# Kernel tuning notes

Measured on AMD Instinct MI355X. Metric: run time of the kernel, lower is better.

Reference implementation:

```python
import jax, jax.numpy as jnp
import numpy as np

B, N, E, H = 16, 512, 256, 8
ALPHA = 0.2  # leaky relu negative slope


def setup_inputs() -> dict:
    key = jax.random.key(0)
    k1, k2, k3, k4, k5, k6 = jax.random.split(key, 6)
    x = jax.random.normal(k1, (B, N, E), dtype=jnp.float32)
    A = (jax.random.uniform(k2, (B, N, N)) < 0.3).astype(jnp.float32)
    s = 1.0 / np.sqrt(E)
    W = jax.random.uniform(k3, (E, E), minval=-s, maxval=s, dtype=jnp.float32)
    bW = jax.random.uniform(k4, (E,), minval=-s, maxval=s, dtype=jnp.float32)
    a = jax.random.uniform(k5, (E, 2 * H), minval=-s, maxval=s, dtype=jnp.float32)
    ba = jax.random.uniform(k6, (2 * H,), minval=-s, maxval=s, dtype=jnp.float32)
    return {"x": x, "A": A, "W": W, "bW": bW, "a": a, "ba": ba}


def reference(x, A, W, bW, a, ba):
    # Wh = W(x): [B, N, E]
    Wh = jnp.einsum("bne,ef->bnf", x, W) + bW
    # attention coefficients: a(Wh) -> [B, N, 2H] -> [B, H, N, 2]
    e12 = (jnp.einsum("bne,eh->bnh", Wh, a) + ba).reshape(B, N, H, 2).transpose(0, 2, 1, 3)
    e = e12[..., 0:1] + jnp.swapaxes(e12[..., 1:2], -2, -1)  # [B, H, N, N]
    # split heads: [B, H, N, D]
    Whh = Wh.reshape(B, N, H, E // H).transpose(0, 2, 1, 3)
    mask = A[:, None, :, :] > 0.5  # [B, H(bcast), N, N]
    neg = jnp.finfo(e.dtype).min
    score = jnp.where(mask, jax.nn.leaky_relu(e, ALPHA), neg)
    att = jax.nn.softmax(score, axis=-1)
    # rows with no neighbors: torch softmax(-inf row) -> nan -> nan_to_num -> 0
    has_nbr = jnp.any(mask, axis=-1, keepdims=True)
    att = jnp.where(has_nbr, att, 0.0)
    out = jnp.einsum("bhij,bhjd->bhid", att, Whh)  # [B, H, N, D]
    out = out.transpose(0, 2, 1, 3).reshape(B, N, E)
    # dropout is identity in eval/reference mode
    return jax.nn.relu(out)
```

## Files before the change

### kernel.cpp

```cpp
#include <hip/hip_runtime.h>
#include <math.h>

#define Bv 16
#define Nv 512
#define Ev 256
#define Hv 8
#define Dv 32
#define LOG2E 1.44269504088896340736f

typedef _Float16 half8 __attribute__((ext_vector_type(8)));
typedef _Float16 half4_t __attribute__((ext_vector_type(4)));
typedef float f32x4 __attribute__((ext_vector_type(4)));

__global__ __launch_bounds__(256) void prep_kernel(const float* __restrict__ W,
                                                   const float* __restrict__ aP,
                                                   const float* __restrict__ bW,
                                                   const float* __restrict__ ba,
                                                   const float* __restrict__ A,
                                                   _Float16* __restrict__ WT,
                                                   float* __restrict__ Wa,
                                                   float* __restrict__ cba,
                                                   unsigned int* __restrict__ Abm) {
    __shared__ float t[32][33];
    const int tid = threadIdx.x;
    const int blk = blockIdx.x;

    if (blk < 64) {
        const int k0 = (blk >> 3) * 32, n0 = (blk & 7) * 32;
        *(float4*)&t[tid >> 3][(tid & 7) * 4] =
            *(const float4*)&W[(size_t)(k0 + (tid >> 3)) * Ev + n0 + (tid & 7) * 4];
        __syncthreads();
        const int nn = tid >> 3, kg = (tid & 7) * 4;
        half4_t hv;
        hv[0] = (_Float16)t[kg + 0][nn];
        hv[1] = (_Float16)t[kg + 1][nn];
        hv[2] = (_Float16)t[kg + 2][nn];
        hv[3] = (_Float16)t[kg + 3][nn];
        *(half4_t*)&WT[(size_t)(n0 + nn) * Ev + k0 + kg] = hv;
    } else if (blk < 80) {
        const int e = (blk - 64) * 16 + (tid >> 4);
        const int c = tid & 15;
        float dot = 0.f;
        for (int k4 = 0; k4 < 64; ++k4) {
            float4 wv = *(const float4*)&W[(size_t)e * Ev + k4 * 4];
            dot += wv.x * aP[(k4 * 4 + 0) * 16 + c];
            dot += wv.y * aP[(k4 * 4 + 1) * 16 + c];
            dot += wv.z * aP[(k4 * 4 + 2) * 16 + c];
            dot += wv.w * aP[(k4 * 4 + 3) * 16 + c];
        }
        Wa[e * 16 + c] = dot;
    } else if (blk == 80) {
        if (tid < 16) {
            float d = ba[tid];
            for (int k = 0; k < Ev; ++k) d += bW[k] * aP[k * 16 + tid];
            cba[tid] = d;
        }
    } else {
        const int ablk = blk - 81;
        const int w = tid >> 6, lane = tid & 63;
        const size_t base = (size_t)ablk * 2048 + w * 512;
        #pragma unroll
        for (int r = 0; r < 8; ++r) {
            const size_t f = base + r * 64 + lane;
            const bool pred = A[f] > 0.5f;
            unsigned long long m = __ballot(pred);
            if (lane == 0) *(unsigned long long*)&Abm[f >> 5] = m;
        }
    }
}

__global__ __launch_bounds__(256) void whT_gemm(const float* __restrict__ x,
                                                const _Float16* __restrict__ WT,
                                                const float* __restrict__ bW,
                                                _Float16* __restrict__ WhT) {
    __shared__ _Float16 xs[64][40];
    __shared__ _Float16 wsT[64][40];
    __shared__ _Float16 ldsTr[64][72];

    const int tid = threadIdx.x;
    const int m0 = blockIdx.x * 64;
    const int n0 = blockIdx.y * 64;
    const int w = tid >> 6;
    const int lane = tid & 63;
    const int row = lane & 15;
    const int strip = lane >> 4;

    f32x4 acc[4] = {{0.f, 0.f, 0.f, 0.f}, {0.f, 0.f, 0.f, 0.f},
                    {0.f, 0.f, 0.f, 0.f}, {0.f, 0.f, 0.f, 0.f}};

    const int sr = tid >> 2;
    const int skg = (tid & 3) * 8;

    for (int k0 = 0; k0 < Ev; k0 += 32) {
        {
            const float* xp = &x[(size_t)(m0 + sr) * Ev + k0 + skg];
            float4 v0 = *(const float4*)xp;
            float4 v1 = *(const float4*)(xp + 4);
            half8 hv;
            hv[0] = (_Float16)v0.x; hv[1] = (_Float16)v0.y;
            hv[2] = (_Float16)v0.z; hv[3] = (_Float16)v0.w;
            hv[4] = (_Float16)v1.x; hv[5] = (_Float16)v1.y;
            hv[6] = (_Float16)v1.z; hv[7] = (_Float16)v1.w;
            *(half8*)&xs[sr][skg] = hv;
        }
        {
            half8 hv = *(const half8*)&WT[(size_t)(n0 + sr) * Ev + k0 + skg];
            *(half8*)&wsT[sr][skg] = hv;
        }
        __syncthreads();

        half8 af = *(const half8*)&xs[w * 16 + row][strip * 8];
        #pragma unroll
        for (int ns = 0; ns < 4; ++ns) {
            half8 bf = *(const half8*)&wsT[ns * 16 + row][strip * 8];
            acc[ns] = __builtin_amdgcn_mfma_f32_16x16x32_f16(af, bf, acc[ns], 0, 0, 0);
        }
        __syncthreads();
    }

    #pragma unroll
    for (int ns = 0; ns < 4; ++ns) {
        const float bias = bW[n0 + ns * 16 + row];
        half4_t hv;
        hv[0] = (_Float16)(acc[ns][0] + bias);
        hv[1] = (_Float16)(acc[ns][1] + bias);
        hv[2] = (_Float16)(acc[ns][2] + bias);
        hv[3] = (_Float16)(acc[ns][3] + bias);
        *(half4_t*)&ldsTr[ns * 16 + row][w * 16 + strip * 4] = hv;
    }
    __syncthreads();

    {
        const int n = tid >> 2, jg = tid & 3;
        uint4 v0 = *(const uint4*)&ldsTr[n][jg * 16];
        uint4 v1 = *(const uint4*)&ldsTr[n][jg * 16 + 8];
        const int ng = n0 + n;
        const int h = ng >> 5, d = ng & 31;
        const int b = m0 >> 9, j0 = m0 & 511;
        _Float16* dst = &WhT[(((size_t)b * Hv + h) * Dv + d) * Nv + j0 + jg * 16];
        *(uint4*)dst = v0;
        *(uint4*)(dst + 8) = v1;
    }
}

__global__ __launch_bounds__(256) void e12_kernel(const float* __restrict__ x,
                                                  const float* __restrict__ Wa,
                                                  const float* __restrict__ cba,
                                                  float* __restrict__ e1,
                                                  float* __restrict__ e2) {
    __shared__ float WaS[Ev][16];
    __shared__ float cbaS[16];

    const int tid = threadIdx.x;
    const int m0 = blockIdx.x * 32;

    #pragma unroll
    for (int u = 0; u < 4; ++u) {
        int f = tid + u * 256;
        *(float4*)&WaS[f >> 2][(f & 3) * 4] = *(const float4*)&Wa[f * 4];
    }
    if (tid < 16) cbaS[tid] = cba[tid];
    __syncthreads();

    const int r = tid >> 3;
    const int q = (tid >> 1) & 3;
    const int kh = tid & 1;
    const int m = m0 + r;

    const float* xr = &x[(size_t)m * Ev + kh * 128];
    float4 acc = {0.f, 0.f, 0.f, 0.f};

    #pragma unroll 8
    for (int it = 0; it < 32; ++it) {
        float4 xv = *(const float4*)&xr[it * 4];
        const int kb = kh * 128 + it * 4;
        float4 w0 = *(const float4*)&WaS[kb + 0][q * 4];
        float4 w1 = *(const float4*)&WaS[kb + 1][q * 4];
        float4 w2 = *(const float4*)&WaS[kb + 2][q * 4];
        float4 w3 = *(const float4*)&WaS[kb + 3][q * 4];
        acc.x += xv.x * w0.x + xv.y * w1.x + xv.z * w2.x + xv.w * w3.x;
        acc.y += xv.x * w0.y + xv.y * w1.y + xv.z * w2.y + xv.w * w3.y;
        acc.z += xv.x * w0.z + xv.y * w1.z + xv.z * w2.z + xv.w * w3.z;
        acc.w += xv.x * w0.w + xv.y * w1.w + xv.z * w2.w + xv.w * w3.w;
    }

    acc.x += __shfl_xor(acc.x, 1);
    acc.y += __shfl_xor(acc.y, 1);
    acc.z += __shfl_xor(acc.z, 1);
    acc.w += __shfl_xor(acc.w, 1);

    if (kh == 0) {
        const int b = m >> 9, i = m & 511;
        #pragma unroll
        for (int cc = 0; cc < 4; ++cc) {
            const int c = q * 4 + cc;
            const float val = ((cc == 0) ? acc.x : (cc == 1) ? acc.y : (cc == 2) ? acc.z : acc.w)
                              + cbaS[c];
            const int h = c >> 1;
            float* dst = (c & 1) ? e2 : e1;
            dst[(((b << 3) + h) << 9) + i] = val;
        }
    }
}

__global__ __launch_bounds__(256) void attn_kernel(const unsigned int* __restrict__ Abm,
                                                   const _Float16* __restrict__ WhT,
                                                   const float* __restrict__ e1g,
                                                   const float* __restrict__ e2g,
                                                   float* __restrict__ out) {
    __shared__ _Float16 whT[Dv * Nv];
    __shared__ float E2pS[Nv];
    __shared__ float E2nS[Nv];

    const int tid = threadIdx.x;
    const int i0 = blockIdx.x * 64;
    const int h = blockIdx.y;
    const int b = blockIdx.z;
    const int bh = (b << 3) + h;

    const _Float16* src = WhT + (size_t)bh * (Dv * Nv);
    #pragma unroll
    for (int u = 0; u < 8; ++u) {
        int f = tid + u * 256;
        int d = f >> 6, blk = f & 63;
        uint4 v = *(const uint4*)(src + d * Nv + blk * 8);
        *(uint4*)&whT[d * Nv + ((blk ^ (d & 7)) * 8)] = v;
    }
    {
        float ea = e2g[(bh << 9) + tid] * LOG2E;
        E2pS[tid] = __builtin_amdgcn_exp2f(ea);
        E2nS[tid] = __builtin_amdgcn_exp2f(0.2f * ea);
        float eb = e2g[(bh << 9) + tid + 256] * LOG2E;
        E2pS[tid + 256] = __builtin_amdgcn_exp2f(eb);
        E2nS[tid + 256] = __builtin_amdgcn_exp2f(0.2f * eb);
    }
    __syncthreads();

    const int w = tid >> 6;
    const int lane = tid & 63;
    const int row = lane & 15;
    const int strip = lane >> 4;
    const int i = i0 + (w << 4) + row;

    const float e1v = e1g[(bh << 9) + i] * LOG2E;
    const float E1p = __builtin_amdgcn_exp2f(e1v);
    const float E1n = __builtin_amdgcn_exp2f(0.2f * e1v);

    const uint4* bmp = (const uint4*)&Abm[((size_t)b * Nv + i) << 4];
    const uint4 bm0 = bmp[0], bm1 = bmp[1], bm2 = bmp[2], bm3 = bmp[3];
    const unsigned int dwarr[16] = {bm0.x, bm0.y, bm0.z, bm0.w,
                                    bm1.x, bm1.y, bm1.z, bm1.w,
                                    bm2.x, bm2.y, bm2.z, bm2.w,
                                    bm3.x, bm3.y, bm3.z, bm3.w};
    const int sh = strip << 3;

    const int d0 = lane & 15;
    const int sw = d0 & 7;
    const _Float16* brow0 = &whT[d0 * Nv];
    const _Float16* brow1 = &whT[(16 + d0) * Nv];

    f32x4 acc0 = {0.f, 0.f, 0.f, 0.f};
    f32x4 acc1 = {0.f, 0.f, 0.f, 0.f};
    float denom = 0.f;

    #pragma unroll
    for (int t = 0; t < 16; ++t) {
        const unsigned int byte_ = (dwarr[t] >> sh) & 0xFFu;
        const float4 p0 = *(const float4*)&E2pS[t * 32 + sh];
        const float4 p1 = *(const float4*)&E2pS[t * 32 + sh + 4];
        const float4 n0 = *(const float4*)&E2nS[t * 32 + sh];
        const float4 n1 = *(const float4*)&E2nS[t * 32 + sh + 4];

        const float q0 = (byte_ & 1u)   ? fmaxf(E1p * p0.x, E1n * n0.x) : 0.f;
        const float q1 = (byte_ & 2u)   ? fmaxf(E1p * p0.y, E1n * n0.y) : 0.f;
        const float q2 = (byte_ & 4u)   ? fmaxf(E1p * p0.z, E1n * n0.z) : 0.f;
        const float q3 = (byte_ & 8u)   ? fmaxf(E1p * p0.w, E1n * n0.w) : 0.f;
        const float q4 = (byte_ & 16u)  ? fmaxf(E1p * p1.x, E1n * n1.x) : 0.f;
        const float q5 = (byte_ & 32u)  ? fmaxf(E1p * p1.y, E1n * n1.y) : 0.f;
        const float q6 = (byte_ & 64u)  ? fmaxf(E1p * p1.z, E1n * n1.z) : 0.f;
        const float q7 = (byte_ & 128u) ? fmaxf(E1p * p1.w, E1n * n1.w) : 0.f;

        denom += ((q0 + q1) + (q2 + q3)) + ((q4 + q5) + (q6 + q7));

        half8 af;
        af[0] = (_Float16)q0; af[1] = (_Float16)q1;
        af[2] = (_Float16)q2; af[3] = (_Float16)q3;
        af[4] = (_Float16)q4; af[5] = (_Float16)q5;
        af[6] = (_Float16)q6; af[7] = (_Float16)q7;

        const int blk = ((t << 2) + strip) ^ sw;
        half8 b0 = *(const half8*)(brow0 + blk * 8);
        half8 b1 = *(const half8*)(brow1 + blk * 8);
        acc0 = __builtin_amdgcn_mfma_f32_16x16x32_f16(af, b0, acc0, 0, 0, 0);
        acc1 = __builtin_amdgcn_mfma_f32_16x16x32_f16(af, b1, acc1, 0, 0, 0);
    }

    denom += __shfl_xor(denom, 16);
    denom += __shfl_xor(denom, 32);

    #pragma unroll
    for (int e = 0; e < 4; ++e) {
        const float dn = __shfl(denom, (strip << 2) + e);
        const float rv = (dn > 0.f) ? (1.f / dn) : 0.f;
        const int orow = i0 + (w << 4) + (strip << 2) + e;
        float* orp = &out[((size_t)b * Nv + orow) * Ev + (h << 5)];
        orp[d0] = fmaxf(acc0[e] * rv, 0.f);
        orp[16 + d0] = fmaxf(acc1[e] * rv, 0.f);
    }
}

extern "C" void kernel_launch(void* const* d_in, const int* in_sizes, int n_in,
                              void* d_out, int out_size, void* d_ws, size_t ws_size,
                              hipStream_t stream) {
    const float* x  = (const float*)d_in[0];
    const float* A  = (const float*)d_in[1];
    const float* W  = (const float*)d_in[2];
    const float* bW = (const float*)d_in[3];
    const float* a  = (const float*)d_in[4];
    const float* ba = (const float*)d_in[5];
    float* out = (float*)d_out;

    char* ws = (char*)d_ws;
    _Float16* WT  = (_Float16*)ws;
    float*    Wa  = (float*)(ws + 131072);
    float*    cba = (float*)(ws + 131072 + 16384);
    _Float16* WhT = (_Float16*)(ws + 131072 + 16384 + 256);
    float*    e1  = (float*)(ws + 131072 + 16384 + 256 + 4194304);
    float*    e2  = e1 + (size_t)Bv * Hv * Nv;
    unsigned int* Abm = (unsigned int*)(e2 + (size_t)Bv * Hv * Nv);

    prep_kernel<<<2129, 256, 0, stream>>>(W, a, bW, ba, A, WT, Wa, cba, Abm);
    whT_gemm<<<dim3(Bv * Nv / 64, Ev / 64), 256, 0, stream>>>(x, WT, bW, WhT);
    e12_kernel<<<dim3(Bv * Nv / 32), 256, 0, stream>>>(x, Wa, cba, e1, e2);
    attn_kernel<<<dim3(Nv / 64, Hv, Bv), 256, 0, stream>>>(Abm, WhT, e1, e2, out);
}
```

Measured before the change: 45.27 us.

## Fuse W transpose and Wh GEMM into prep kernel; double rows per attention wave

Merges the separate weight-transpose and Wh GEMM launches into one fused prep kernel. Each GEMM block now loads and transposes its 256x64 slice of W straight into LDS as fp16, which removes one kernel launch and the WT round trip through global memory. The attention kernel now gives each wave 32 rows instead of 16, so the staged WhT tile and E2 values are reused across twice as many rows with half as many blocks. The cost is a larger LDS footprint and redundant W reads in the prep kernel, more registers in attention, and lower block count and occupancy.

```diff
diff --git a/kernel.cpp b/kernel.cpp
--- a/kernel.cpp
+++ b/kernel.cpp
@@ -12,33 +12,96 @@
 typedef _Float16 half4_t __attribute__((ext_vector_type(4)));
 typedef float f32x4 __attribute__((ext_vector_type(4)));
 
-__global__ __launch_bounds__(256) void prep_kernel(const float* __restrict__ W,
-                                                   const float* __restrict__ aP,
-                                                   const float* __restrict__ bW,
-                                                   const float* __restrict__ ba,
-                                                   const float* __restrict__ A,
-                                                   _Float16* __restrict__ WT,
-                                                   float* __restrict__ Wa,
-                                                   float* __restrict__ cba,
-                                                   unsigned int* __restrict__ Abm) {
-    __shared__ float t[32][33];
+__global__ __launch_bounds__(256) void fused_pre(const float* __restrict__ x,
+                                                 const float* __restrict__ W,
+                                                 const float* __restrict__ bW,
+                                                 const float* __restrict__ aP,
+                                                 const float* __restrict__ ba,
+                                                 const float* __restrict__ A,
+                                                 _Float16* __restrict__ WhT,
+                                                 float* __restrict__ Wa,
+                                                 float* __restrict__ cba,
+                                                 unsigned int* __restrict__ Abm) {
+    __shared__ _Float16 Wp[64][264];
+    __shared__ _Float16 xs[64][40];
+    __shared__ _Float16 ldsTr[64][72];
+
     const int tid = threadIdx.x;
     const int blk = blockIdx.x;
 
-    if (blk < 64) {
-        const int k0 = (blk >> 3) * 32, n0 = (blk & 7) * 32;
-        *(float4*)&t[tid >> 3][(tid & 7) * 4] =
-            *(const float4*)&W[(size_t)(k0 + (tid >> 3)) * Ev + n0 + (tid & 7) * 4];
+    if (blk < 512) {
+        const int m0 = (blk >> 2) * 64;
+        const int n0 = (blk & 3) * 64;
+        const int w = tid >> 6;
+        const int lane = tid & 63;
+        const int row = lane & 15;
+        const int strip = lane >> 4;
+
+        {
+            const float* wrow = &W[(size_t)tid * Ev + n0];
+            #pragma unroll
+            for (int u = 0; u < 16; ++u) {
+                float4 v = *(const float4*)&wrow[u * 4];
+                Wp[u * 4 + 0][tid] = (_Float16)v.x;
+                Wp[u * 4 + 1][tid] = (_Float16)v.y;
+                Wp[u * 4 + 2][tid] = (_Float16)v.z;
+                Wp[u * 4 + 3][tid] = (_Float16)v.w;
+            }
+        }
+
+        f32x4 acc[4] = {{0.f, 0.f, 0.f, 0.f}, {0.f, 0.f, 0.f, 0.f},
+                        {0.f, 0.f, 0.f, 0.f}, {0.f, 0.f, 0.f, 0.f}};
+        const int sr = tid >> 2;
+        const int skg = (tid & 3) * 8;
+
+        for (int k0 = 0; k0 < Ev; k0 += 32) {
+            {
+                const float* xp = &x[(size_t)(m0 + sr) * Ev + k0 + skg];
+                float4 v0 = *(const float4*)xp;
+                float4 v1 = *(const float4*)(xp + 4);
+                half8 hv;
+                hv[0] = (_Float16)v0.x; hv[1] = (_Float16)v0.y;
+                hv[2] = (_Float16)v0.z; hv[3] = (_Float16)v0.w;
+                hv[4] = (_Float16)v1.x; hv[5] = (_Float16)v1.y;
+                hv[6] = (_Float16)v1.z; hv[7] = (_Float16)v1.w;
+                *(half8*)&xs[sr][skg] = hv;
+            }
+            __syncthreads();
+
+            half8 af = *(const half8*)&xs[w * 16 + row][strip * 8];
+            #pragma unroll
+            for (int ns = 0; ns < 4; ++ns) {
+                half8 bf = *(const half8*)&Wp[ns * 16 + row][k0 + strip * 8];
+                acc[ns] = __builtin_amdgcn_mfma_f32_16x16x32_f16(af, bf, acc[ns], 0, 0, 0);
+            }
+            __syncthreads();
+        }
+
+        #pragma unroll
+        for (int ns = 0; ns < 4; ++ns) {
+            const float bias = bW[n0 + ns * 16 + row];
+            half4_t hv;
+            hv[0] = (_Float16)(acc[ns][0] + bias);
+            hv[1] = (_Float16)(acc[ns][1] + bias);
+            hv[2] = (_Float16)(acc[ns][2] + bias);
+            hv[3] = (_Float16)(acc[ns][3] + bias);
+            *(half4_t*)&ldsTr[ns * 16 + row][w * 16 + strip * 4] = hv;
+        }
         __syncthreads();
-        const int nn = tid >> 3, kg = (tid & 7) * 4;
-        half4_t hv;
-        hv[0] = (_Float16)t[kg + 0][nn];
-        hv[1] = (_Float16)t[kg + 1][nn];
-        hv[2] = (_Float16)t[kg + 2][nn];
-        hv[3] = (_Float16)t[kg + 3][nn];
-        *(half4_t*)&WT[(size_t)(n0 + nn) * Ev + k0 + kg] = hv;
-    } else if (blk < 80) {
-        const int e = (blk - 64) * 16 + (tid >> 4);
+
+        {
+            const int n = tid >> 2, jg = tid & 3;
+            uint4 v0 = *(const uint4*)&ldsTr[n][jg * 16];
+            uint4 v1 = *(const uint4*)&ldsTr[n][jg * 16 + 8];
+            const int ng = n0 + n;
+            const int h = ng >> 5, d = ng & 31;
+            const int b = m0 >> 9, j0 = m0 & 511;
+            _Float16* dst = &WhT[(((size_t)b * Hv + h) * Dv + d) * Nv + j0 + jg * 16];
+            *(uint4*)dst = v0;
+            *(uint4*)(dst + 8) = v1;
+        }
+    } else if (blk < 528) {
+        const int e = (blk - 512) * 16 + (tid >> 4);
         const int c = tid & 15;
         float dot = 0.f;
         for (int k4 = 0; k4 < 64; ++k4) {
@@ -49,14 +112,14 @@
             dot += wv.w * aP[(k4 * 4 + 3) * 16 + c];
         }
         Wa[e * 16 + c] = dot;
-    } else if (blk == 80) {
+    } else if (blk == 528) {
         if (tid < 16) {
             float d = ba[tid];
             for (int k = 0; k < Ev; ++k) d += bW[k] * aP[k * 16 + tid];
             cba[tid] = d;
         }
     } else {
-        const int ablk = blk - 81;
+        const int ablk = blk - 529;
         const int w = tid >> 6, lane = tid & 63;
         const size_t base = (size_t)ablk * 2048 + w * 512;
         #pragma unroll
@@ -66,80 +129,6 @@
             unsigned long long m = __ballot(pred);
             if (lane == 0) *(unsigned long long*)&Abm[f >> 5] = m;
         }
-    }
-}
-
-__global__ __launch_bounds__(256) void whT_gemm(const float* __restrict__ x,
-                                                const _Float16* __restrict__ WT,
-                                                const float* __restrict__ bW,
-                                                _Float16* __restrict__ WhT) {
-    __shared__ _Float16 xs[64][40];
-    __shared__ _Float16 wsT[64][40];
-    __shared__ _Float16 ldsTr[64][72];
-
-    const int tid = threadIdx.x;
-    const int m0 = blockIdx.x * 64;
-    const int n0 = blockIdx.y * 64;
-    const int w = tid >> 6;
-    const int lane = tid & 63;
-    const int row = lane & 15;
-    const int strip = lane >> 4;
-
-    f32x4 acc[4] = {{0.f, 0.f, 0.f, 0.f}, {0.f, 0.f, 0.f, 0.f},
-                    {0.f, 0.f, 0.f, 0.f}, {0.f, 0.f, 0.f, 0.f}};
-
-    const int sr = tid >> 2;
-    const int skg = (tid & 3) * 8;
-
-    for (int k0 = 0; k0 < Ev; k0 += 32) {
-        {
-            const float* xp = &x[(size_t)(m0 + sr) * Ev + k0 + skg];
-            float4 v0 = *(const float4*)xp;
-            float4 v1 = *(const float4*)(xp + 4);
-            half8 hv;
-            hv[0] = (_Float16)v0.x; hv[1] = (_Float16)v0.y;
-            hv[2] = (_Float16)v0.z; hv[3] = (_Float16)v0.w;
-            hv[4] = (_Float16)v1.x; hv[5] = (_Float16)v1.y;
-            hv[6] = (_Float16)v1.z; hv[7] = (_Float16)v1.w;
-            *(half8*)&xs[sr][skg] = hv;
-        }
-        {
-            half8 hv = *(const half8*)&WT[(size_t)(n0 + sr) * Ev + k0 + skg];
-            *(half8*)&wsT[sr][skg] = hv;
-        }
-        __syncthreads();
-
-        half8 af = *(const half8*)&xs[w * 16 + row][strip * 8];
-        #pragma unroll
-        for (int ns = 0; ns < 4; ++ns) {
-            half8 bf = *(const half8*)&wsT[ns * 16 + row][strip * 8];
-            acc[ns] = __builtin_amdgcn_mfma_f32_16x16x32_f16(af, bf, acc[ns], 0, 0, 0);
-        }
-        __syncthreads();
-    }
-
-    #pragma unroll
-    for (int ns = 0; ns < 4; ++ns) {
-        const float bias = bW[n0 + ns * 16 + row];
-        half4_t hv;
-        hv[0] = (_Float16)(acc[ns][0] + bias);
-        hv[1] = (_Float16)(acc[ns][1] + bias);
-        hv[2] = (_Float16)(acc[ns][2] + bias);
-        hv[3] = (_Float16)(acc[ns][3] + bias);
-        *(half4_t*)&ldsTr[ns * 16 + row][w * 16 + strip * 4] = hv;
-    }
-    __syncthreads();
-
-    {
-        const int n = tid >> 2, jg = tid & 3;
-        uint4 v0 = *(const uint4*)&ldsTr[n][jg * 16];
-        uint4 v1 = *(const uint4*)&ldsTr[n][jg * 16 + 8];
-        const int ng = n0 + n;
-        const int h = ng >> 5, d = ng & 31;
-        const int b = m0 >> 9, j0 = m0 & 511;
-        _Float16* dst = &WhT[(((size_t)b * Hv + h) * Dv + d) * Nv + j0 + jg * 16];
-        *(uint4*)dst = v0;
-        *(uint4*)(dst + 8) = v1;
     }
 }
 
@@ -213,7 +202,7 @@
     __shared__ float E2nS[Nv];
 
     const int tid = threadIdx.x;
-    const int i0 = blockIdx.x * 64;
+    const int i0 = blockIdx.x * 128;
     const int h = blockIdx.y;
     const int b = blockIdx.z;
     const int bh = (b << 3) + h;
@@ -222,9 +211,9 @@
     #pragma unroll
     for (int u = 0; u < 8; ++u) {
         int f = tid + u * 256;
-        int d = f >> 6, blk = f & 63;
-        uint4 v = *(const uint4*)(src + d * Nv + blk * 8);
-        *(uint4*)&whT[d * Nv + ((blk ^ (d & 7)) * 8)] = v;
+        int d = f >> 6, bq = f & 63;
+        uint4 v = *(const uint4*)(src + d * Nv + bq * 8);
+        *(uint4*)&whT[d * Nv + ((bq ^ (d & 7)) * 8)] = v;
     }
     {
         float ea = e2g[(bh << 9) + tid] * LOG2E;
@@ -240,72 +229,104 @@
     const int lane = tid & 63;
     const int row = lane & 15;
     const int strip = lane >> 4;
-    const int i = i0 + (w << 4) + row;
-
-    const float e1v = e1g[(bh << 9) + i] * LOG2E;
-    const float E1p = __builtin_amdgcn_exp2f(e1v);
-    const float E1n = __builtin_amdgcn_exp2f(0.2f * e1v);
-
-    const uint4* bmp = (const uint4*)&Abm[((size_t)b * Nv + i) << 4];
-    const uint4 bm0 = bmp[0], bm1 = bmp[1], bm2 = bmp[2], bm3 = bmp[3];
-    const unsigned int dwarr[16] = {bm0.x, bm0.y, bm0.z, bm0.w,
-                                    bm1.x, bm1.y, bm1.z, bm1.w,
-                                    bm2.x, bm2.y, bm2.z, bm2.w,
-                                    bm3.x, bm3.y, bm3.z, bm3.w};
+    const int iA = i0 + (w << 5) + row;
+    const int iB = iA + 16;
+
+    const float e1A = e1g[(bh << 9) + iA] * LOG2E;
+    const float e1B = e1g[(bh << 9) + iB] * LOG2E;
+    const float E1pA = __builtin_amdgcn_exp2f(e1A);
+    const float E1nA = __builtin_amdgcn_exp2f(0.2f * e1A);
+    const float E1pB = __builtin_amdgcn_exp2f(e1B);
+    const float E1nB = __builtin_amdgcn_exp2f(0.2f * e1B);
+
+    const uint4* bpA = (const uint4*)&Abm[((size_t)b * Nv + iA) << 4];
+    const uint4 mA0 = bpA[0], mA1 = bpA[1], mA2 = bpA[2], mA3 = bpA[3];
+    const uint4* bpB = (const uint4*)&Abm[((size_t)b * Nv + iB) << 4];
+    const uint4 mB0 = bpB[0], mB1 = bpB[1], mB2 = bpB[2], mB3 = bpB[3];
+
     const int sh = strip << 3;
-
     const int d0 = lane & 15;
     const int sw = d0 & 7;
     const _Float16* brow0 = &whT[d0 * Nv];
     const _Float16* brow1 = &whT[(16 + d0) * Nv];
 
-    f32x4 acc0 = {0.f, 0.f, 0.f, 0.f};
-    f32x4 acc1 = {0.f, 0.f, 0.f, 0.f};
-    float denom = 0.f;
+    f32x4 accA0 = {0.f, 0.f, 0.f, 0.f}, accA1 = accA0;
+    f32x4 accB0 = accA0, accB1 = accA0;
+    float denA = 0.f, denB = 0.f;
 
     #pragma unroll
     for (int t = 0; t < 16; ++t) {
-        const unsigned int byte_ = (dwarr[t] >> sh) & 0xFFu;
+        const uint4 mqA = (t >> 2) == 0 ? mA0 : (t >> 2) == 1 ? mA1 : (t >> 2) == 2 ? mA2 : mA3;
+        const uint4 mqB = (t >> 2) == 0 ? mB0 : (t >> 2) == 1 ? mB1 : (t >> 2) == 2 ? mB2 : mB3;
+        const unsigned int dwA = (t & 3) == 0 ? mqA.x : (t & 3) == 1 ? mqA.y : (t & 3) == 2 ? mqA.z : mqA.w;
+        const unsigned int dwB = (t & 3) == 0 ? mqB.x : (t & 3) == 1 ? mqB.y : (t & 3) == 2 ? mqB.z : mqB.w;
+        const unsigned int byA = (dwA >> sh) & 0xFFu;
+        const unsigned int byB = (dwB >> sh) & 0xFFu;
+
         const float4 p0 = *(const float4*)&E2pS[t * 32 + sh];
         const float4 p1 = *(const float4*)&E2pS[t * 32 + sh + 4];
         const float4 n0 = *(const float4*)&E2nS[t * 32 + sh];
         const float4 n1 = *(const float4*)&E2nS[t * 32 + sh + 4];
 
-        const float q0 = (byte_ & 1u)   ? fmaxf(E1p * p0.x, E1n * n0.x) : 0.f;
-        const float q1 = (byte_ & 2u)   ? fmaxf(E1p * p0.y, E1n * n0.y) : 0.f;
-        const float q2 = (byte_ & 4u)   ? fmaxf(E1p * p0.z, E1n * n0.z) : 0.f;
-        const float q3 = (byte_ & 8u)   ? fmaxf(E1p * p0.w, E1n * n0.w) : 0.f;
-        const float q4 = (byte_ & 16u)  ? fmaxf(E1p * p1.x, E1n * n1.x) : 0.f;
-        const float q5 = (byte_ & 32u)  ? fmaxf(E1p * p1.y, E1n * n1.y) : 0.f;
-        const float q6 = (byte_ & 64u)  ? fmaxf(E1p * p1.z, E1n * n1.z) : 0.f;
-        const float q7 = (byte_ & 128u) ? fmaxf(E1p * p1.w, E1n * n1.w) : 0.f;
-
-        denom += ((q0 + q1) + (q2 + q3)) + ((q4 + q5) + (q6 + q7));
-
-        half8 af;
-        af[0] = (_Float16)q0; af[1] = (_Float16)q1;
-        af[2] = (_Float16)q2; af[3] = (_Float16)q3;
-        af[4] = (_Float16)q4; af[5] = (_Float16)q5;
-        af[6] = (_Float16)q6; af[7] = (_Float16)q7;
-
-        const int blk = ((t << 2) + strip) ^ sw;
-        half8 b0 = *(const half8*)(brow0 + blk * 8);
-        half8 b1 = *(const half8*)(brow1 + blk * 8);
-        acc0 = __builtin_amdgcn_mfma_f32_16x16x32_f16(af, b0, acc0, 0, 0, 0);
-        acc1 = __builtin_amdgcn_mfma_f32_16x16x32_f16(af, b1, acc1, 0, 0, 0);
-    }
-
-    denom += __shfl_xor(denom, 16);
-    denom += __shfl_xor(denom, 32);
+        const float qA0 = (byA & 1u)   ? fmaxf(E1pA * p0.x, E1nA * n0.x) : 0.f;
+        const float qA1 = (byA & 2u)   ? fmaxf(E1pA * p0.y, E1nA * n0.y) : 0.f;
+        const float qA2 = (byA & 4u)   ? fmaxf(E1pA * p0.z, E1nA * n0.z) : 0.f;
+        const float qA3 = (byA & 8u)   ? fmaxf(E1pA * p0.w, E1nA * n0.w) : 0.f;
+        const float qA4 = (byA & 16u)  ? fmaxf(E1pA * p1.x, E1nA * n1.x) : 0.f;
+        const float qA5 = (byA & 32u)  ? fmaxf(E1pA * p1.y, E1nA * n1.y) : 0.f;
+        const float qA6 = (byA & 64u)  ? fmaxf(E1pA * p1.z, E1nA * n1.z) : 0.f;
+        const float qA7 = (byA & 128u) ? fmaxf(E1pA * p1.w, E1nA * n1.w) : 0.f;
+        const float qB0 = (byB & 1u)   ? fmaxf(E1pB * p0.x, E1nB * n0.x) : 0.f;
+        const float qB1 = (byB & 2u)   ? fmaxf(E1pB * p0.y, E1nB * n0.y) : 0.f;
+        const float qB2 = (byB & 4u)   ? fmaxf(E1pB * p0.z, E1nB * n0.z) : 0.f;
+        const float qB3 = (byB & 8u)   ? fmaxf(E1pB * p0.w, E1nB * n0.w) : 0.f;
+        const float qB4 = (byB & 16u)  ? fmaxf(E1pB * p1.x, E1nB * n1.x) : 0.f;
+        const float qB5 = (byB & 32u)  ? fmaxf(E1pB * p1.y, E1nB * n1.y) : 0.f;
+        const float qB6 = (byB & 64u)  ? fmaxf(E1pB * p1.z, E1nB * n1.z) : 0.f;
+        const float qB7 = (byB & 128u) ? fmaxf(E1pB * p1.w, E1nB * n1.w) : 0.f;
+
+        denA += ((qA0 + qA1) + (qA2 + qA3)) + ((qA4 + qA5) + (qA6 + qA7));
+        denB += ((qB0 + qB1) + (qB2 + qB3)) + ((qB4 + qB5) + (qB6 + qB7));
+
+        half8 afA, afB;
+        afA[0] = (_Float16)qA0; afA[1] = (_Float16)qA1;
+        afA[2] = (_Float16)qA2; afA[3] = (_Float16)qA3;
+        afA[4] = (_Float16)qA4; afA[5] = (_Float16)qA5;
+        afA[6] = (_Float16)qA6; afA[7] = (_Float16)qA7;
+        afB[0] = (_Float16)qB0; afB[1] = (_Float16)qB1;
+        afB[2] = (_Float16)qB2; afB[3] = (_Float16)qB3;
+        afB[4] = (_Float16)qB4; afB[5] = (_Float16)qB5;
+        afB[6] = (_Float16)qB6; afB[7] = (_Float16)qB7;
+
+        const int bq = ((t << 2) + strip) ^ sw;
+        half8 b0 = *(const half8*)(brow0 + bq * 8);
+        half8 b1 = *(const half8*)(brow1 + bq * 8);
+        accA0 = __builtin_amdgcn_mfma_f32_16x16x32_f16(afA, b0, accA0, 0, 0, 0);
+        accA1 = __builtin_amdgcn_mfma_f32_16x16x32_f16(afA, b1, accA1, 0, 0, 0);
+        accB0 = __builtin_amdgcn_mfma_f32_16x16x32_f16(afB, b0, accB0, 0, 0, 0);
+        accB1 = __builtin_amdgcn_mfma_f32_16x16x32_f16(afB, b1, accB1, 0, 0, 0);
+    }
+
+    denA += __shfl_xor(denA, 16);
+    denA += __shfl_xor(denA, 32);
+    denB += __shfl_xor(denB, 16);
+    denB += __shfl_xor(denB, 32);
 
     #pragma unroll
     for (int e = 0; e < 4; ++e) {
-        const float dn = __shfl(denom, (strip << 2) + e);
-        const float rv = (dn > 0.f) ? (1.f / dn) : 0.f;
-        const int orow = i0 + (w << 4) + (strip << 2) + e;
-        float* orp = &out[((size_t)b * Nv + orow) * Ev + (h << 5)];
-        orp[d0] = fmaxf(acc0[e] * rv, 0.f);
-        orp[16 + d0] = fmaxf(acc1[e] * rv, 0.f);
+        const float dnA = __shfl(denA, (strip << 2) + e);
+        const float rvA = (dnA > 0.f) ? (1.f / dnA) : 0.f;
+        const int orA = i0 + (w << 5) + (strip << 2) + e;
+        float* opA = &out[((size_t)b * Nv + orA) * Ev + (h << 5)];
+        opA[d0] = fmaxf(accA0[e] * rvA, 0.f);
+        opA[16 + d0] = fmaxf(accA1[e] * rvA, 0.f);
+
+        const float dnB = __shfl(denB, (strip << 2) + e);
+        const float rvB = (dnB > 0.f) ? (1.f / dnB) : 0.f;
+        const int orB = orA + 16;
+        float* opB = &out[((size_t)b * Nv + orB) * Ev + (h << 5)];
+        opB[d0] = fmaxf(accB0[e] * rvB, 0.f);
+        opB[16 + d0] = fmaxf(accB1[e] * rvB, 0.f);
     }
 }
 
@@ -321,16 +342,14 @@
     float* out = (float*)d_out;
 
     char* ws = (char*)d_ws;
-    _Float16* WT  = (_Float16*)ws;
-    float*    Wa  = (float*)(ws + 131072);
-    float*    cba = (float*)(ws + 131072 + 16384);
-    _Float16* WhT = (_Float16*)(ws + 131072 + 16384 + 256);
-    float*    e1  = (float*)(ws + 131072 + 16384 + 256 + 4194304);
-    float*    e2  = e1 + (size_t)Bv * Hv * Nv;
-    unsigned int* Abm = (unsigned int*)(e2 + (size_t)Bv * Hv * Nv);
-
-    prep_kernel<<<2129, 256, 0, stream>>>(W, a, bW, ba, A, WT, Wa, cba, Abm);
-    whT_gemm<<<dim3(Bv * Nv / 64, Ev / 64), 256, 0, stream>>>(x, WT, bW, WhT);
+    float*        Wa  = (float*)(ws);
+    float*        cba = (float*)(ws + 16384);
+    float*        e1  = (float*)(ws + 32768);
+    float*        e2  = (float*)(ws + 294912);
+    unsigned int* Abm = (unsigned int*)(ws + 557056);
+    _Float16*     WhT = (_Float16*)(ws + 1572864);
+
+    fused_pre<<<2577, 256, 0, stream>>>(x, W, bW, a, ba, A, WhT, Wa, cba, Abm);
     e12_kernel<<<dim3(Bv * Nv / 32), 256, 0, stream>>>(x, Wa, cba, e1, e2);
-    attn_kernel<<<dim3(Nv / 64, Hv, Bv), 256, 0, stream>>>(Abm, WhT, e1, e2, out);
+    attn_kernel<<<dim3(Nv / 128, Hv, Bv), 256, 0, stream>>>(Abm, WhT, e1, e2, out);
 }
```

Result: faster. 42.75 us (-5.6%).
